# Kernel optimization log

Hardware: AMD Instinct MI355X
Metric: run time of the kernel (lower is better)

The kernel has to match this reference:

```python
import jax, jax.numpy as jnp
import numpy as np

B, T, C, H = 8, 2048, 1024, 64

def setup_inputs() -> dict:
    key = jax.random.key(0)
    k1, k2, k3, k4 = jax.random.split(key, 4)
    x = jax.random.normal(k1, (B, T, C), dtype=jnp.float32)
    s = 1.0 / np.sqrt(C)
    Wq = jax.random.normal(k2, (C, H), dtype=jnp.float32) * s
    Wk = jax.random.normal(k3, (C, H), dtype=jnp.float32) * s
    Wv = jax.random.normal(k4, (C, H), dtype=jnp.float32) * s
    return {"x": x, "Wq": Wq, "Wk": Wk, "Wv": Wv}

def reference(x, Wq, Wk, Wv):
    # single-head causal attention; note: scale uses sqrt(n_emb)=sqrt(C), as in source
    q = jnp.einsum('btc,ch->bth', x, Wq)
    k = jnp.einsum('btc,ch->bth', x, Wk)
    v = jnp.einsum('btc,ch->bth', x, Wv)
    wei = jnp.einsum('bth,bsh->bts', q, k) / jnp.sqrt(jnp.float32(C))  # [B,T,T]
    causal = jnp.tril(jnp.ones((T, T), dtype=bool))
    wei = jnp.where(causal, wei, jnp.float32(-jnp.inf))
    wei = jax.nn.softmax(wei, axis=-1)
    out = jnp.einsum('bts,bsh->bth', wei, v)  # [B,T,H]
    return out
```

## Files before the change

### kernel.cpp

```cpp
#include <hip/hip_runtime.h>

#define BT_ (8 * 2048)
#define T_  2048
#define H_  64

__global__ __launch_bounds__(256) void qkv_proj(
    const float* __restrict__ x,
    const float* __restrict__ Wq,
    const float* __restrict__ Wk,
    const float* __restrict__ Wv,
    float* __restrict__ qkv) {
  __shared__ float xT[32][68];
  __shared__ float wl[32][196];

  const int tid = threadIdx.x;
  const int tx = tid & 15;
  const int ty = tid >> 4;
  const int row0 = blockIdx.x * 64;

  float acc[4][12];
#pragma unroll
  for (int r = 0; r < 4; ++r)
#pragma unroll
    for (int c = 0; c < 12; ++c) acc[r][c] = 0.f;

  for (int kc = 0; kc < 1024; kc += 32) {
#pragma unroll
    for (int i = 0; i < 2; ++i) {
      int idx = tid + i * 256;
      int r = idx >> 3;
      int k4 = (idx & 7) * 4;
      const float4 v = *reinterpret_cast<const float4*>(
          &x[(size_t)(row0 + r) * 1024 + kc + k4]);
      xT[k4 + 0][r] = v.x;
      xT[k4 + 1][r] = v.y;
      xT[k4 + 2][r] = v.z;
      xT[k4 + 3][r] = v.w;
    }
    {
      const float* wp[3] = {Wq, Wk, Wv};
#pragma unroll
      for (int m = 0; m < 3; ++m) {
#pragma unroll
        for (int i = 0; i < 2; ++i) {
          int idx = tid + i * 256;
          int r = idx >> 4;
          int h4 = (idx & 15) * 4;
          const float4 v = *reinterpret_cast<const float4*>(
              &wp[m][(size_t)(kc + r) * 64 + h4]);
          *reinterpret_cast<float4*>(&wl[r][m * 64 + h4]) = v;
        }
      }
    }
    __syncthreads();

#pragma unroll
    for (int kk = 0; kk < 32; ++kk) {
      const float4 xv = *reinterpret_cast<const float4*>(&xT[kk][ty * 4]);
      const float4 w0 = *reinterpret_cast<const float4*>(&wl[kk][tx * 12 + 0]);
      const float4 w1 = *reinterpret_cast<const float4*>(&wl[kk][tx * 12 + 4]);
      const float4 w2 = *reinterpret_cast<const float4*>(&wl[kk][tx * 12 + 8]);
      const float xr[4] = {xv.x, xv.y, xv.z, xv.w};
      const float wr[12] = {w0.x, w0.y, w0.z, w0.w, w1.x, w1.y, w1.z, w1.w,
                            w2.x, w2.y, w2.z, w2.w};
#pragma unroll
      for (int r = 0; r < 4; ++r)
#pragma unroll
        for (int c = 0; c < 12; ++c)
          acc[r][c] = fmaf(xr[r], wr[c], acc[r][c]);
    }
    __syncthreads();
  }

#pragma unroll
  for (int r = 0; r < 4; ++r) {
#pragma unroll
    for (int g = 0; g < 3; ++g) {
      const int col = tx * 12 + g * 4;
      const int m = col >> 6;
      const int h = col & 63;
      float4 v = make_float4(acc[r][g * 4 + 0], acc[r][g * 4 + 1],
                             acc[r][g * 4 + 2], acc[r][g * 4 + 3]);
      *reinterpret_cast<float4*>(
          &qkv[(size_t)m * BT_ * H_ + (size_t)(row0 + ty * 4 + r) * H_ + h]) = v;
    }
  }
}

__global__ __launch_bounds__(256) void attn_fwd(
    const float* __restrict__ qkv, float* __restrict__ out) {
  __shared__ float qT[64][36];
  __shared__ float kT[64][68];
  __shared__ float vl[64][68];
  __shared__ float pT[64][36];

  const int tid = threadIdx.x;
  const int tx = tid & 15;
  const int ty = tid >> 4;
  const int b  = blockIdx.x & 7;
  const int qt = 63 - (blockIdx.x >> 3);
  const int r0 = qt * 32;

  const float* Q = qkv;
  const float* K = qkv + (size_t)BT_ * H_;
  const float* V = qkv + (size_t)2 * BT_ * H_;

#pragma unroll
  for (int i = 0; i < 2; ++i) {
    int idx = tid + i * 256;
    int r = idx >> 4;
    int h4 = (idx & 15) * 4;
    float4 v = *reinterpret_cast<const float4*>(
        &Q[((size_t)b * T_ + r0 + r) * H_ + h4]);
    qT[h4 + 0][r] = v.x * 0.03125f;
    qT[h4 + 1][r] = v.y * 0.03125f;
    qT[h4 + 2][r] = v.z * 0.03125f;
    qT[h4 + 3][r] = v.w * 0.03125f;
  }

  float m0 = -1e30f, m1 = -1e30f, l0 = 0.f, l1 = 0.f;
  float o0[4] = {0, 0, 0, 0}, o1[4] = {0, 0, 0, 0};

  const int nkt = qt / 2 + 1;
  for (int kt = 0; kt < nkt; ++kt) {
#pragma unroll
    for (int i = 0; i < 4; ++i) {
      int idx = tid + i * 256;
      int j = idx >> 4;
      int h4 = (idx & 15) * 4;
      size_t g = ((size_t)b * T_ + kt * 64 + j) * H_ + h4;
      float4 kv = *reinterpret_cast<const float4*>(&K[g]);
      kT[h4 + 0][j] = kv.x;
      kT[h4 + 1][j] = kv.y;
      kT[h4 + 2][j] = kv.z;
      kT[h4 + 3][j] = kv.w;
      *reinterpret_cast<float4*>(&vl[j][h4]) =
          *reinterpret_cast<const float4*>(&V[g]);
    }
    __syncthreads();

    float s0[4] = {0, 0, 0, 0}, s1[4] = {0, 0, 0, 0};
#pragma unroll
    for (int h = 0; h < 64; ++h) {
      float2 qv = *reinterpret_cast<const float2*>(&qT[h][ty * 2]);
      float4 kv = *reinterpret_cast<const float4*>(&kT[h][tx * 4]);
      const float kr[4] = {kv.x, kv.y, kv.z, kv.w};
#pragma unroll
      for (int c = 0; c < 4; ++c) {
        s0[c] = fmaf(qv.x, kr[c], s0[c]);
        s1[c] = fmaf(qv.y, kr[c], s1[c]);
      }
    }

    if (kt == nkt - 1) {
      const int rg = r0 + ty * 2;
#pragma unroll
      for (int c = 0; c < 4; ++c) {
        const int jg = kt * 64 + tx * 4 + c;
        if (jg > rg)     s0[c] = -1e30f;
        if (jg > rg + 1) s1[c] = -1e30f;
      }
    }

    float mt0 = fmaxf(fmaxf(s0[0], s0[1]), fmaxf(s0[2], s0[3]));
    float mt1 = fmaxf(fmaxf(s1[0], s1[1]), fmaxf(s1[2], s1[3]));
#pragma unroll
    for (int d = 1; d < 16; d <<= 1) {
      mt0 = fmaxf(mt0, __shfl_xor(mt0, d));
      mt1 = fmaxf(mt1, __shfl_xor(mt1, d));
    }
    const float mn0 = fmaxf(m0, mt0), mn1 = fmaxf(m1, mt1);
    const float a0 = __expf(m0 - mn0), a1 = __expf(m1 - mn1);
    float p0[4], p1[4], sum0 = 0.f, sum1 = 0.f;
#pragma unroll
    for (int c = 0; c < 4; ++c) {
      p0[c] = __expf(s0[c] - mn0);
      p1[c] = __expf(s1[c] - mn1);
      sum0 += p0[c];
      sum1 += p1[c];
    }
#pragma unroll
    for (int d = 1; d < 16; d <<= 1) {
      sum0 += __shfl_xor(sum0, d);
      sum1 += __shfl_xor(sum1, d);
    }
    l0 = l0 * a0 + sum0;
    l1 = l1 * a1 + sum1;
    m0 = mn0;
    m1 = mn1;
#pragma unroll
    for (int c = 0; c < 4; ++c) {
      o0[c] *= a0;
      o1[c] *= a1;
    }

#pragma unroll
    for (int c = 0; c < 4; ++c) {
      pT[tx * 4 + c][ty * 2 + 0] = p0[c];
      pT[tx * 4 + c][ty * 2 + 1] = p1[c];
    }
    __syncthreads();

#pragma unroll
    for (int j = 0; j < 64; ++j) {
      float2 pv = *reinterpret_cast<const float2*>(&pT[j][ty * 2]);
      float4 vv = *reinterpret_cast<const float4*>(&vl[j][tx * 4]);
      const float vr[4] = {vv.x, vv.y, vv.z, vv.w};
#pragma unroll
      for (int c = 0; c < 4; ++c) {
        o0[c] = fmaf(pv.x, vr[c], o0[c]);
        o1[c] = fmaf(pv.y, vr[c], o1[c]);
      }
    }
    __syncthreads();
  }

  const float inv0 = 1.0f / l0, inv1 = 1.0f / l1;
  const size_t orow = ((size_t)b * T_ + r0 + ty * 2) * H_ + tx * 4;
  *reinterpret_cast<float4*>(&out[orow]) =
      make_float4(o0[0] * inv0, o0[1] * inv0, o0[2] * inv0, o0[3] * inv0);
  *reinterpret_cast<float4*>(&out[orow + H_]) =
      make_float4(o1[0] * inv1, o1[1] * inv1, o1[2] * inv1, o1[3] * inv1);
}

extern "C" void kernel_launch(void* const* d_in, const int* in_sizes, int n_in,
                              void* d_out, int out_size, void* d_ws,
                              size_t ws_size, hipStream_t stream) {
  const float* x  = (const float*)d_in[0];
  const float* Wq = (const float*)d_in[1];
  const float* Wk = (const float*)d_in[2];
  const float* Wv = (const float*)d_in[3];
  float* ws  = (float*)d_ws;
  float* out = (float*)d_out;

  qkv_proj<<<256, 256, 0, stream>>>(x, Wq, Wk, Wv, ws);
  attn_fwd<<<512, 256, 0, stream>>>(ws, out);
}
```

Baseline: 316.3 us.

## Add atomic-ticket persistent scheduling to attention, shuffle P and shrink projection tiles

```diff
diff --git a/kernel.cpp b/kernel.cpp
--- a/kernel.cpp
+++ b/kernel.cpp
@@ -3,6 +3,7 @@
 #define BT_ (8 * 2048)
 #define T_  2048
 #define H_  64
+#define NTICK 512
 
 __global__ __launch_bounds__(256) void qkv_proj(
     const float* __restrict__ x,
@@ -10,26 +11,24 @@
     const float* __restrict__ Wk,
     const float* __restrict__ Wv,
     float* __restrict__ qkv) {
-  __shared__ float xT[32][68];
+  __shared__ float xT[32][33];
   __shared__ float wl[32][196];
 
   const int tid = threadIdx.x;
   const int tx = tid & 15;
   const int ty = tid >> 4;
-  const int row0 = blockIdx.x * 64;
-
-  float acc[4][12];
-#pragma unroll
-  for (int r = 0; r < 4; ++r)
+  const int row0 = blockIdx.x * 32;
+
+  float acc[2][12];
+#pragma unroll
+  for (int r = 0; r < 2; ++r)
 #pragma unroll
     for (int c = 0; c < 12; ++c) acc[r][c] = 0.f;
 
   for (int kc = 0; kc < 1024; kc += 32) {
-#pragma unroll
-    for (int i = 0; i < 2; ++i) {
-      int idx = tid + i * 256;
-      int r = idx >> 3;
-      int k4 = (idx & 7) * 4;
+    {
+      int r = tid >> 3;
+      int k4 = (tid & 7) * 4;
       const float4 v = *reinterpret_cast<const float4*>(
           &x[(size_t)(row0 + r) * 1024 + kc + k4]);
       xT[k4 + 0][r] = v.x;
@@ -56,15 +55,15 @@
 
 #pragma unroll
     for (int kk = 0; kk < 32; ++kk) {
-      const float4 xv = *reinterpret_cast<const float4*>(&xT[kk][ty * 4]);
+      const float2 xv = *reinterpret_cast<const float2*>(&xT[kk][ty * 2]);
       const float4 w0 = *reinterpret_cast<const float4*>(&wl[kk][tx * 12 + 0]);
       const float4 w1 = *reinterpret_cast<const float4*>(&wl[kk][tx * 12 + 4]);
       const float4 w2 = *reinterpret_cast<const float4*>(&wl[kk][tx * 12 + 8]);
-      const float xr[4] = {xv.x, xv.y, xv.z, xv.w};
+      const float xr[2] = {xv.x, xv.y};
       const float wr[12] = {w0.x, w0.y, w0.z, w0.w, w1.x, w1.y, w1.z, w1.w,
                             w2.x, w2.y, w2.z, w2.w};
 #pragma unroll
-      for (int r = 0; r < 4; ++r)
+      for (int r = 0; r < 2; ++r)
 #pragma unroll
         for (int c = 0; c < 12; ++c)
           acc[r][c] = fmaf(xr[r], wr[c], acc[r][c]);
@@ -73,7 +72,7 @@
   }
 
 #pragma unroll
-  for (int r = 0; r < 4; ++r) {
+  for (int r = 0; r < 2; ++r) {
 #pragma unroll
     for (int g = 0; g < 3; ++g) {
       const int col = tx * 12 + g * 4;
@@ -82,145 +81,151 @@
       float4 v = make_float4(acc[r][g * 4 + 0], acc[r][g * 4 + 1],
                              acc[r][g * 4 + 2], acc[r][g * 4 + 3]);
       *reinterpret_cast<float4*>(
-          &qkv[(size_t)m * BT_ * H_ + (size_t)(row0 + ty * 4 + r) * H_ + h]) = v;
+          &qkv[(size_t)m * BT_ * H_ + (size_t)(row0 + ty * 2 + r) * H_ + h]) = v;
     }
   }
 }
 
 __global__ __launch_bounds__(256) void attn_fwd(
-    const float* __restrict__ qkv, float* __restrict__ out) {
-  __shared__ float qT[64][36];
-  __shared__ float kT[64][68];
-  __shared__ float vl[64][68];
-  __shared__ float pT[64][36];
+    const float* __restrict__ qkv, float* __restrict__ out,
+    unsigned int* __restrict__ ctr) {
+  __shared__ float qT[64][33];
+  __shared__ float kT[64][65];
+  __shared__ float vl[64][65];
+  __shared__ unsigned int sticket;
 
   const int tid = threadIdx.x;
   const int tx = tid & 15;
   const int ty = tid >> 4;
-  const int b  = blockIdx.x & 7;
-  const int qt = 63 - (blockIdx.x >> 3);
-  const int r0 = qt * 32;
+  const int lane = tid & 63;
 
   const float* Q = qkv;
   const float* K = qkv + (size_t)BT_ * H_;
   const float* V = qkv + (size_t)2 * BT_ * H_;
 
-#pragma unroll
-  for (int i = 0; i < 2; ++i) {
-    int idx = tid + i * 256;
-    int r = idx >> 4;
-    int h4 = (idx & 15) * 4;
-    float4 v = *reinterpret_cast<const float4*>(
-        &Q[((size_t)b * T_ + r0 + r) * H_ + h4]);
-    qT[h4 + 0][r] = v.x * 0.03125f;
-    qT[h4 + 1][r] = v.y * 0.03125f;
-    qT[h4 + 2][r] = v.z * 0.03125f;
-    qT[h4 + 3][r] = v.w * 0.03125f;
+  while (true) {
+    if (tid == 0) sticket = atomicAdd(ctr, 1u);
+    __syncthreads();
+    const unsigned int t = sticket;
+    if (t >= (unsigned)NTICK) break;
+    const int b = (int)(t & 7);
+    const int qt = 63 - (int)(t >> 3);
+    const int r0 = qt * 32;
+
+#pragma unroll
+    for (int i = 0; i < 2; ++i) {
+      int idx = tid + i * 256;
+      int r = idx >> 4;
+      int h4 = (idx & 15) * 4;
+      float4 v = *reinterpret_cast<const float4*>(
+          &Q[((size_t)b * T_ + r0 + r) * H_ + h4]);
+      qT[h4 + 0][r] = v.x * 0.03125f;
+      qT[h4 + 1][r] = v.y * 0.03125f;
+      qT[h4 + 2][r] = v.z * 0.03125f;
+      qT[h4 + 3][r] = v.w * 0.03125f;
+    }
+
+    float m0 = -1e30f, m1 = -1e30f, l0 = 0.f, l1 = 0.f;
+    float o0[4] = {0, 0, 0, 0}, o1[4] = {0, 0, 0, 0};
+
+    const int nkt = qt / 2 + 1;
+    for (int kt = 0; kt < nkt; ++kt) {
+#pragma unroll
+      for (int i = 0; i < 4; ++i) {
+        int idx = tid + i * 256;
+        int j = idx >> 4;
+        int h4 = (idx & 15) * 4;
+        size_t g = ((size_t)b * T_ + kt * 64 + j) * H_ + h4;
+        float4 kv = *reinterpret_cast<const float4*>(&K[g]);
+        kT[h4 + 0][j] = kv.x;
+        kT[h4 + 1][j] = kv.y;
+        kT[h4 + 2][j] = kv.z;
+        kT[h4 + 3][j] = kv.w;
+        *reinterpret_cast<float4*>(&vl[j][h4]) =
+            *reinterpret_cast<const float4*>(&V[g]);
+      }
+      __syncthreads();
+
+      float s0[4] = {0, 0, 0, 0}, s1[4] = {0, 0, 0, 0};
+#pragma unroll
+      for (int h = 0; h < 64; ++h) {
+        float2 qv = *reinterpret_cast<const float2*>(&qT[h][ty * 2]);
+        float4 kv = *reinterpret_cast<const float4*>(&kT[h][tx * 4]);
+        const float kr[4] = {kv.x, kv.y, kv.z, kv.w};
+#pragma unroll
+        for (int c = 0; c < 4; ++c) {
+          s0[c] = fmaf(qv.x, kr[c], s0[c]);
+          s1[c] = fmaf(qv.y, kr[c], s1[c]);
+        }
+      }
+
+      if (kt == nkt - 1) {
+        const int rg = r0 + ty * 2;
+#pragma unroll
+        for (int c = 0; c < 4; ++c) {
+          const int jg = kt * 64 + tx * 4 + c;
+          if (jg > rg)     s0[c] = -1e30f;
+          if (jg > rg + 1) s1[c] = -1e30f;
+        }
+      }
+
+      float mt0 = fmaxf(fmaxf(s0[0], s0[1]), fmaxf(s0[2], s0[3]));
+      float mt1 = fmaxf(fmaxf(s1[0], s1[1]), fmaxf(s1[2], s1[3]));
+#pragma unroll
+      for (int d = 1; d < 16; d <<= 1) {
+        mt0 = fmaxf(mt0, __shfl_xor(mt0, d));
+        mt1 = fmaxf(mt1, __shfl_xor(mt1, d));
+      }
+      const float mn0 = fmaxf(m0, mt0), mn1 = fmaxf(m1, mt1);
+      const float a0 = __expf(m0 - mn0), a1 = __expf(m1 - mn1);
+      float p0[4], p1[4], sum0 = 0.f, sum1 = 0.f;
+#pragma unroll
+      for (int c = 0; c < 4; ++c) {
+        p0[c] = __expf(s0[c] - mn0);
+        p1[c] = __expf(s1[c] - mn1);
+        sum0 += p0[c];
+        sum1 += p1[c];
+      }
+#pragma unroll
+      for (int d = 1; d < 16; d <<= 1) {
+        sum0 += __shfl_xor(sum0, d);
+        sum1 += __shfl_xor(sum1, d);
+      }
+      l0 = l0 * a0 + sum0;
+      l1 = l1 * a1 + sum1;
+      m0 = mn0;
+      m1 = mn1;
+#pragma unroll
+      for (int c = 0; c < 4; ++c) {
+        o0[c] *= a0;
+        o1[c] *= a1;
+      }
+
+#pragma unroll 8
+      for (int j = 0; j < 64; ++j) {
+        const int src = (lane & 48) | (j >> 2);
+        const float pj0 = __shfl(p0[j & 3], src, 64);
+        const float pj1 = __shfl(p1[j & 3], src, 64);
+        const float4 vv = *reinterpret_cast<const float4*>(&vl[j][tx * 4]);
+        o0[0] = fmaf(pj0, vv.x, o0[0]);
+        o0[1] = fmaf(pj0, vv.y, o0[1]);
+        o0[2] = fmaf(pj0, vv.z, o0[2]);
+        o0[3] = fmaf(pj0, vv.w, o0[3]);
+        o1[0] = fmaf(pj1, vv.x, o1[0]);
+        o1[1] = fmaf(pj1, vv.y, o1[1]);
+        o1[2] = fmaf(pj1, vv.z, o1[2]);
+        o1[3] = fmaf(pj1, vv.w, o1[3]);
+      }
+      __syncthreads();
+    }
+
+    const float inv0 = 1.0f / l0, inv1 = 1.0f / l1;
+    const size_t orow = ((size_t)b * T_ + r0 + ty * 2) * H_ + tx * 4;
+    *reinterpret_cast<float4*>(&out[orow]) =
+        make_float4(o0[0] * inv0, o0[1] * inv0, o0[2] * inv0, o0[3] * inv0);
+    *reinterpret_cast<float4*>(&out[orow + H_]) =
+        make_float4(o1[0] * inv1, o1[1] * inv1, o1[2] * inv1, o1[3] * inv1);
   }
-
-  float m0 = -1e30f, m1 = -1e30f, l0 = 0.f, l1 = 0.f;
-  float o0[4] = {0, 0, 0, 0}, o1[4] = {0, 0, 0, 0};
-
-  const int nkt = qt / 2 + 1;
-  for (int kt = 0; kt < nkt; ++kt) {
-#pragma unroll
-    for (int i = 0; i < 4; ++i) {
-      int idx = tid + i * 256;
-      int j = idx >> 4;
-      int h4 = (idx & 15) * 4;
-      size_t g = ((size_t)b * T_ + kt * 64 + j) * H_ + h4;
-      float4 kv = *reinterpret_cast<const float4*>(&K[g]);
-      kT[h4 + 0][j] = kv.x;
-      kT[h4 + 1][j] = kv.y;
-      kT[h4 + 2][j] = kv.z;
-      kT[h4 + 3][j] = kv.w;
-      *reinterpret_cast<float4*>(&vl[j][h4]) =
-          *reinterpret_cast<const float4*>(&V[g]);
-    }
-    __syncthreads();
-
-    float s0[4] = {0, 0, 0, 0}, s1[4] = {0, 0, 0, 0};
-#pragma unroll
-    for (int h = 0; h < 64; ++h) {
-      float2 qv = *reinterpret_cast<const float2*>(&qT[h][ty * 2]);
-      float4 kv = *reinterpret_cast<const float4*>(&kT[h][tx * 4]);
-      const float kr[4] = {kv.x, kv.y, kv.z, kv.w};
-#pragma unroll
-      for (int c = 0; c < 4; ++c) {
-        s0[c] = fmaf(qv.x, kr[c], s0[c]);
-        s1[c] = fmaf(qv.y, kr[c], s1[c]);
-      }
-    }
-
-    if (kt == nkt - 1) {
-      const int rg = r0 + ty * 2;
-#pragma unroll
-      for (int c = 0; c < 4; ++c) {
-        const int jg = kt * 64 + tx * 4 + c;
-        if (jg > rg)     s0[c] = -1e30f;
-        if (jg > rg + 1) s1[c] = -1e30f;
-      }
-    }
-
-    float mt0 = fmaxf(fmaxf(s0[0], s0[1]), fmaxf(s0[2], s0[3]));
-    float mt1 = fmaxf(fmaxf(s1[0], s1[1]), fmaxf(s1[2], s1[3]));
-#pragma unroll
-    for (int d = 1; d < 16; d <<= 1) {
-      mt0 = fmaxf(mt0, __shfl_xor(mt0, d));
-      mt1 = fmaxf(mt1, __shfl_xor(mt1, d));
-    }
-    const float mn0 = fmaxf(m0, mt0), mn1 = fmaxf(m1, mt1);
-    const float a0 = __expf(m0 - mn0), a1 = __expf(m1 - mn1);
-    float p0[4], p1[4], sum0 = 0.f, sum1 = 0.f;
-#pragma unroll
-    for (int c = 0; c < 4; ++c) {
-      p0[c] = __expf(s0[c] - mn0);
-      p1[c] = __expf(s1[c] - mn1);
-      sum0 += p0[c];
-      sum1 += p1[c];
-    }
-#pragma unroll
-    for (int d = 1; d < 16; d <<= 1) {
-      sum0 += __shfl_xor(sum0, d);
-      sum1 += __shfl_xor(sum1, d);
-    }
-    l0 = l0 * a0 + sum0;
-    l1 = l1 * a1 + sum1;
-    m0 = mn0;
-    m1 = mn1;
-#pragma unroll
-    for (int c = 0; c < 4; ++c) {
-      o0[c] *= a0;
-      o1[c] *= a1;
-    }
-
-#pragma unroll
-    for (int c = 0; c < 4; ++c) {
-      pT[tx * 4 + c][ty * 2 + 0] = p0[c];
-      pT[tx * 4 + c][ty * 2 + 1] = p1[c];
-    }
-    __syncthreads();
-
-#pragma unroll
-    for (int j = 0; j < 64; ++j) {
-      float2 pv = *reinterpret_cast<const float2*>(&pT[j][ty * 2]);
-      float4 vv = *reinterpret_cast<const float4*>(&vl[j][tx * 4]);
-      const float vr[4] = {vv.x, vv.y, vv.z, vv.w};
-#pragma unroll
-      for (int c = 0; c < 4; ++c) {
-        o0[c] = fmaf(pv.x, vr[c], o0[c]);
-        o1[c] = fmaf(pv.y, vr[c], o1[c]);
-      }
-    }
-    __syncthreads();
-  }
-
-  const float inv0 = 1.0f / l0, inv1 = 1.0f / l1;
-  const size_t orow = ((size_t)b * T_ + r0 + ty * 2) * H_ + tx * 4;
-  *reinterpret_cast<float4*>(&out[orow]) =
-      make_float4(o0[0] * inv0, o0[1] * inv0, o0[2] * inv0, o0[3] * inv0);
-  *reinterpret_cast<float4*>(&out[orow + H_]) =
-      make_float4(o1[0] * inv1, o1[1] * inv1, o1[2] * inv1, o1[3] * inv1);
 }
 
 extern "C" void kernel_launch(void* const* d_in, const int* in_sizes, int n_in,
@@ -232,7 +237,10 @@
   const float* Wv = (const float*)d_in[3];
   float* ws  = (float*)d_ws;
   float* out = (float*)d_out;
-
-  qkv_proj<<<256, 256, 0, stream>>>(x, Wq, Wk, Wv, ws);
-  attn_fwd<<<512, 256, 0, stream>>>(ws, out);
+  unsigned int* ctr =
+      (unsigned int*)((char*)d_ws + (size_t)3 * BT_ * H_ * sizeof(float));
+
+  qkv_proj<<<512, 256, 0, stream>>>(x, Wq, Wk, Wv, ws);
+  hipMemsetAsync(ctr, 0, sizeof(unsigned int), stream);
+  attn_fwd<<<768, 256, 0, stream>>>(ws, out, ctr);
 }
```

Result: slower. 420.7 us (+33.0%).
